# Kernel tuning notes

Measured on AMD Instinct MI355X. Metric: run time of the kernel, lower is better.

Reference implementation:

```python
import jax, jax.numpy as jnp
import numpy as np

B, S, D, H = 2, 2048, 1024, 16
HD = D // H          # 64
NREF = HD // 2       # 32 Householder reflections
BLOCK = 128          # flex_attention block granularity
ROPE_BASE = 10000.0


def setup_inputs() -> dict:
    key = jax.random.key(0)
    ks = jax.random.split(key, 12)
    x = jax.random.normal(ks[0], (B, S, D), jnp.float32)
    # block-causal block mask (flex_attention block_mask analogue)
    nb = S // BLOCK
    bm = jnp.tril(jnp.ones((nb, nb), bool))
    mask = jnp.repeat(jnp.repeat(bm, BLOCK, axis=0), BLOCK, axis=1)  # [S,S]
    s = lambda fan: fan ** -0.5
    vs = jax.random.normal(ks[1], (NREF, HD), jnp.float32) * 0.02
    w_qkv = jax.random.normal(ks[2], (D, 3 * D), jnp.float32) * s(D)
    w_out = jax.random.normal(ks[3], (D, D), jnp.float32) * s(D)
    w_gate = jax.random.normal(ks[4], (D, D), jnp.float32) * s(D)
    b_gate = jnp.zeros((D,), jnp.float32)
    w_mlp_gate = jax.random.normal(ks[5], (D, 8 * D), jnp.float32) * s(D)
    b_mlp_gate = jnp.zeros((8 * D,), jnp.float32)
    w_mlp_out = jax.random.normal(ks[6], (4 * D, D), jnp.float32) * s(4 * D)
    b_mlp_out = jnp.zeros((D,), jnp.float32)
    return dict(x=x, mask=mask, grid_size=S, vs=vs, w_qkv=w_qkv, w_out=w_out,
                w_gate=w_gate, b_gate=b_gate, w_mlp_gate=w_mlp_gate,
                b_mlp_gate=b_mlp_gate, w_mlp_out=w_mlp_out, b_mlp_out=b_mlp_out)


def rmsnorm(x):
    return x * jax.lax.rsqrt(jnp.mean(x * x, axis=-1, keepdims=True) + 1e-6)


def householder_matrix(vs):
    # Q = prod_i (I - 2 v_i v_i^T / |v_i|^2), applied sequentially as in torch loop
    def body(Q, v):
        vn = jnp.sum(v * v) + 1e-8
        return Q - (2.0 / vn) * jnp.outer(v, v @ Q), None
    Q0 = jnp.eye(HD, dtype=vs.dtype)
    Q, _ = jax.lax.scan(body, Q0, vs)
    return Q


def rope_tables(seq_len, dtype):
    inv_freq = 1.0 / (ROPE_BASE ** (jnp.arange(0, HD, 2, dtype=jnp.float32) / HD))
    ang = jnp.arange(seq_len, dtype=jnp.float32)[:, None] * inv_freq  # [S, HD/2]
    ang = jnp.concatenate([ang, ang], axis=-1)                        # [S, HD]
    return jnp.cos(ang).astype(dtype), jnp.sin(ang).astype(dtype)


def rotate_half(x):
    x1, x2 = jnp.split(x, 2, axis=-1)
    return jnp.concatenate([-x2, x1], axis=-1)


def reference(x, mask, grid_size, vs, w_qkv, w_out, w_gate, b_gate,
              w_mlp_gate, b_mlp_gate, w_mlp_out, b_mlp_out):
    del grid_size  # positions derived from sequence length
    resid = x
    h = rmsnorm(x)
    qkv = h @ w_qkv                                # [B,S,3D]
    q, k, v = jnp.split(qkv, 3, axis=-1)
    to_heads = lambda t: t.reshape(B, S, H, HD).transpose(0, 2, 1, 3)  # [B,H,S,hd]
    q, k, v = to_heads(q), to_heads(k), to_heads(v)

    # RnRoPE: inverse Householder rotation, rope, forward Householder rotation
    Q = householder_matrix(vs)                     # [hd,hd]
    q = q @ Q.T
    k = k @ Q.T
    cos, sin = rope_tables(S, x.dtype)             # [S,hd]
    cos = cos[None, None]; sin = sin[None, None]
    q = q * cos + rotate_half(q) * sin
    k = k * cos + rotate_half(k) * sin
    q = q @ Q
    k = k @ Q

    # block-sparse attention (mask realized as boolean [S,S])
    scores = jnp.einsum('bhqd,bhkd->bhqk', q, k) / jnp.sqrt(jnp.asarray(HD, x.dtype))
    scores = jnp.where(mask[None, None], scores, jnp.asarray(-1e30, x.dtype))
    attn = jnp.einsum('bhqk,bhkd->bhqd', jax.nn.softmax(scores, axis=-1), v)
    attn = attn.transpose(0, 2, 1, 3).reshape(B, S, D)
    attn = attn @ w_out

    gate = jax.nn.sigmoid(attn @ w_gate + b_gate)
    x = resid + attn * gate

    resid = x
    gv = rmsnorm(x) @ w_mlp_gate + b_mlp_gate      # [B,S,8D]
    g, val = jnp.split(gv, 2, axis=-1)
    x = resid + (val * jax.nn.gelu(g, approximate=False)) @ w_mlp_out + b_mlp_out
    return x
```

## Files before the change

kernel.cpp:

```cpp
#include <hip/hip_runtime.h>
#include <hip/hip_bf16.h>
#include <math.h>

#define BT 2
#define SEQ 2048
#define DIM 1024
#define NH 16
#define HD 64
#define NTOK (BT*SEQ)

typedef __attribute__((ext_vector_type(4))) float floatx4;
typedef __attribute__((ext_vector_type(8))) short shortx8;
typedef __attribute__((ext_vector_type(4))) short shortx4;

#define GLL16(gp, lp) __builtin_amdgcn_global_load_lds( \
    (const __attribute__((address_space(1))) unsigned int*)(const void*)(gp), \
    (__attribute__((address_space(3))) unsigned int*)(void*)(lp), 16, 0, 0)

__device__ __forceinline__ float bf2f(unsigned short u) {
    unsigned int x = ((unsigned int)u) << 16;
    return __builtin_bit_cast(float, x);
}
__device__ __forceinline__ unsigned short f2bf(float f) {
    unsigned int x = __builtin_bit_cast(unsigned int, f);
    unsigned int lsb = (x >> 16) & 1u;
    x += 0x7fffu + lsb;
    return (unsigned short)(x >> 16);
}
__device__ __forceinline__ float ldin_f(const void* p, size_t i, int isbf) {
    return isbf ? bf2f(((const unsigned short*)p)[i]) : ((const float*)p)[i];
}

__global__ void detect_kernel(const unsigned short* __restrict__ x, int* __restrict__ flag) {
    __shared__ int cnt;
    if (threadIdx.x == 0) cnt = 0;
    __syncthreads();
    unsigned short u = x[(size_t)threadIdx.x * 2];
    int e = (u >> 7) & 0xFF;
    if (e >= 100 && e <= 140) atomicAdd(&cnt, 1);
    __syncthreads();
    if (threadIdx.x == 0) *flag = (cnt >= 192) ? 1 : 0;
}

__global__ void transpose_any(const void* __restrict__ in,
                              unsigned short* __restrict__ out, int R, int C,
                              const int* __restrict__ flagp) {
    int isbf = *flagp;
    __shared__ unsigned short tile[32][33];
    int c0 = blockIdx.x * 32, r0 = blockIdx.y * 32;
    int tx = threadIdx.x, ty = threadIdx.y;
#pragma unroll
    for (int i = 0; i < 4; i++) {
        size_t idx = (size_t)(r0 + ty + i * 8) * C + c0 + tx;
        tile[ty + i * 8][tx] = isbf ? ((const unsigned short*)in)[idx]
                                    : f2bf(((const float*)in)[idx]);
    }
    __syncthreads();
#pragma unroll
    for (int i = 0; i < 4; i++)
        out[(size_t)(c0 + ty + i * 8) * R + r0 + tx] = tile[tx][ty + i * 8];
}

__global__ __launch_bounds__(64) void householder_kernel(const void* __restrict__ vs,
                                                         float* __restrict__ Qg,
                                                         const int* __restrict__ flagp) {
    int isbf = *flagp;
    __shared__ float vsh[64];
    int j = threadIdx.x;
    float Qc[64];
#pragma unroll
    for (int i = 0; i < 64; i++) Qc[i] = (i == j) ? 1.f : 0.f;
    for (int r = 0; r < 32; r++) {
        vsh[j] = ldin_f(vs, r * 64 + j, isbf);
        __syncthreads();
        float va[64];
#pragma unroll
        for (int i = 0; i < 64; i++) va[i] = vsh[i];
        float vn0 = 0.f, vn1 = 0.f, vn2 = 0.f, vn3 = 0.f;
        float t0 = 0.f, t1 = 0.f, t2 = 0.f, t3 = 0.f;
#pragma unroll
        for (int i = 0; i < 16; i++) {
            vn0 += va[4 * i + 0] * va[4 * i + 0];
            vn1 += va[4 * i + 1] * va[4 * i + 1];
            vn2 += va[4 * i + 2] * va[4 * i + 2];
            vn3 += va[4 * i + 3] * va[4 * i + 3];
            t0 += va[4 * i + 0] * Qc[4 * i + 0];
            t1 += va[4 * i + 1] * Qc[4 * i + 1];
            t2 += va[4 * i + 2] * Qc[4 * i + 2];
            t3 += va[4 * i + 3] * Qc[4 * i + 3];
        }
        float vn = (vn0 + vn1) + (vn2 + vn3) + 1e-8f;
        float t = (t0 + t1) + (t2 + t3);
        float c = (2.f / vn) * t;
#pragma unroll
        for (int i = 0; i < 64; i++) Qc[i] -= c * va[i];
        __syncthreads();
    }
#pragma unroll
    for (int i = 0; i < 64; i++) Qg[i * 64 + j] = Qc[i];
}

__global__ __launch_bounds__(256) void rotate_wqkv(unsigned short* __restrict__ wT,
                                                   const float* __restrict__ Qg) {
    __shared__ float Qs[64][64];
    __shared__ unsigned short tile[64][128];
    int bid = blockIdx.x;
    int row0 = (bid >> 3) * 64;
    int col0 = (bid & 7) * 128;
    int t = threadIdx.x;
#pragma unroll
    for (int i = 0; i < 16; i++) {
        int idx = i * 256 + t;
        Qs[idx >> 6][idx & 63] = Qg[idx];
    }
#pragma unroll
    for (int i = 0; i < 8; i++) {
        int e = i * 256 + t;
        int r = e >> 5, cg = (e & 31) * 4;
        *(shortx4*)&tile[r][cg] = *(const shortx4*)&wT[(size_t)(row0 + r) * 1024 + col0 + cg];
    }
    __syncthreads();
    int ib = t >> 5;
    int c = (t & 31) * 4;
    float acc[8][4];
#pragma unroll
    for (int rr = 0; rr < 8; rr++)
#pragma unroll
        for (int cx = 0; cx < 4; cx++) acc[rr][cx] = 0.f;
    for (int j = 0; j < 64; j++) {
        float t0 = bf2f(tile[j][c]);
        float t1 = bf2f(tile[j][c + 1]);
        float t2 = bf2f(tile[j][c + 2]);
        float t3 = bf2f(tile[j][c + 3]);
#pragma unroll
        for (int rr = 0; rr < 8; rr++) {
            float qv = Qs[rr * 8 + ib][j];
            acc[rr][0] += qv * t0;
            acc[rr][1] += qv * t1;
            acc[rr][2] += qv * t2;
            acc[rr][3] += qv * t3;
        }
    }
#pragma unroll
    for (int rr = 0; rr < 8; rr++) {
        int i = rr * 8 + ib;
        shortx4 o4;
#pragma unroll
        for (int cx = 0; cx < 4; cx++) o4[cx] = (short)f2bf(acc[rr][cx]);
        *(shortx4*)&wT[(size_t)(row0 + i) * 1024 + col0 + c] = o4;
    }
}

__global__ void rope_table(float* __restrict__ tab) {
    int idx = blockIdx.x * 256 + threadIdx.x;
    int s = idx >> 5, fi = idx & 31;
    float invf = __expf(-(float)fi * (9.210340371976184f / 32.f));
    float ang = (float)s * invf;
    tab[2 * idx]     = cosf(ang);
    tab[2 * idx + 1] = sinf(ang);
}

__global__ __launch_bounds__(256) void rmsnorm2(const void* __restrict__ x,
                                                unsigned short* __restrict__ h,
                                                const int* __restrict__ flagp) {
    int isbf = flagp ? *flagp : 1;
    __shared__ float red[256];
    int row = blockIdx.x, t = threadIdx.x;
    size_t base = (size_t)row * DIM;
    float v[4];
    float ss = 0.f;
#pragma unroll
    for (int i = 0; i < 4; i++) {
        v[i] = ldin_f(x, base + t + 256 * i, isbf);
        ss += v[i] * v[i];
    }
    red[t] = ss;
    __syncthreads();
    for (int s = 128; s > 0; s >>= 1) {
        if (t < s) red[t] += red[t + s];
        __syncthreads();
    }
    float rs = rsqrtf(red[0] * (1.f / 1024.f) + 1e-6f);
#pragma unroll
    for (int i = 0; i < 4; i++) h[base + t + 256 * i] = f2bf(v[i] * rs);
}

template<int MODE>
__global__ __launch_bounds__(256) void gemm_bt(const unsigned short* __restrict__ A,
                                               const unsigned short* __restrict__ Bt,
                                               void* __restrict__ C,
                                               const void* __restrict__ bias,
                                               const unsigned short* __restrict__ resid,
                                               const void* __restrict__ xin,
                                               const int* __restrict__ flagp,
                                               int M, int N, int K) {
    __shared__ __align__(16) unsigned short As[2][128][64];
    __shared__ __align__(16) unsigned short Bs[2][64][64];
    int isbf = flagp ? *flagp : 1;
    int tile = (blockIdx.x & 7) * (gridDim.x >> 3) + (blockIdx.x >> 3);
    int nbn = N >> 6;
    int m0 = (tile / nbn) * 128;
    int n0 = (tile % nbn) * 64;
    int t = threadIdx.x;
    int lane = t & 63;
    int w = t >> 6;
    int wr = (w >> 1) * 64;
    int wc = (w & 1) * 32;
    int lr = lane & 15;
    int kg = lane >> 4;
    int l8 = lane >> 3, s8 = lane & 7;
    int segswz = (s8 ^ l8) * 8;
    int cs0 = ((kg)     ^ (lr & 7)) * 8;
    int cs1 = ((4 + kg) ^ (lr & 7)) * 8;

    floatx4 acc[4][2];
#pragma unroll
    for (int i = 0; i < 4; i++)
#pragma unroll
        for (int j = 0; j < 2; j++) acc[i][j] = (floatx4){0.f, 0.f, 0.f, 0.f};

    int rbase = w * 8 + l8;
    const unsigned short* aP0 = A + (size_t)(m0 + rbase +  0) * K + segswz;
    const unsigned short* aP1 = A + (size_t)(m0 + rbase + 32) * K + segswz;
    const unsigned short* aP2 = A + (size_t)(m0 + rbase + 64) * K + segswz;
    const unsigned short* aP3 = A + (size_t)(m0 + rbase + 96) * K + segswz;
    const unsigned short* bP0 = Bt + (size_t)(n0 + rbase +  0) * K + segswz;
    const unsigned short* bP1 = Bt + (size_t)(n0 + rbase + 32) * K + segswz;

    auto STAGE = [&](int s, int B) {
        int off = s * 64;
        GLL16(aP0 + off, &As[B][w * 8 +  0][0]);
        GLL16(aP1 + off, &As[B][w * 8 + 32][0]);
        GLL16(aP2 + off, &As[B][w * 8 + 64][0]);
        GLL16(aP3 + off, &As[B][w * 8 + 96][0]);
        GLL16(bP0 + off, &Bs[B][w * 8 +  0][0]);
        GLL16(bP1 + off, &Bs[B][w * 8 + 32][0]);
    };
    auto MM = [&](int B) {
        shortx8 af[4][2], bf[2][2];
#pragma unroll
        for (int i = 0; i < 4; i++) {
            af[i][0] = *(const shortx8*)&As[B][wr + i * 16 + lr][cs0];
            af[i][1] = *(const shortx8*)&As[B][wr + i * 16 + lr][cs1];
        }
#pragma unroll
        for (int j = 0; j < 2; j++) {
            bf[j][0] = *(const shortx8*)&Bs[B][wc + j * 16 + lr][cs0];
            bf[j][1] = *(const shortx8*)&Bs[B][wc + j * 16 + lr][cs1];
        }
#pragma unroll
        for (int i = 0; i < 4; i++)
#pragma unroll
            for (int j = 0; j < 2; j++) {
                acc[i][j] = __builtin_amdgcn_mfma_f32_16x16x32_bf16(af[i][0], bf[j][0], acc[i][j], 0, 0, 0);
                acc[i][j] = __builtin_amdgcn_mfma_f32_16x16x32_bf16(af[i][1], bf[j][1], acc[i][j], 0, 0, 0);
            }
    };

    int NS = K >> 6;
    STAGE(0, 0);
    __syncthreads();
    for (int s = 0; s < NS; s += 2) {
        if (s + 1 < NS) STAGE(s + 1, 1);
        MM(0);
        __syncthreads();
        if (s + 1 < NS) {
            if (s + 2 < NS) STAGE(s + 2, 0);
            MM(1);
            __syncthreads();
        }
    }
#pragma unroll
    for (int i = 0; i < 4; i++) {
#pragma unroll
        for (int j = 0; j < 2; j++) {
            int col = n0 + wc + j * 16 + lr;
            int rb = m0 + wr + i * 16 + kg * 4;
            float bv = bias ? ldin_f(bias, col, isbf) : 0.f;
#pragma unroll
            for (int r = 0; r < 4; r++) {
                float val = acc[i][j][r] + bv;
                size_t oidx = (size_t)(rb + r) * N + col;
                if constexpr (MODE == 0) {
                    ((unsigned short*)C)[oidx] = f2bf(val);
                } else if constexpr (MODE == 1) {
                    ((float*)C)[oidx] = val + bf2f(resid[oidx]);
                } else {
                    float a = bf2f(resid[oidx]);
                    float sg = 1.f / (1.f + __expf(-val));
                    ((unsigned short*)C)[oidx] = f2bf(ldin_f(xin, oidx, isbf) + a * sg);
                }
            }
        }
    }
}

__global__ __launch_bounds__(256) void gemm_glu(const unsigned short* __restrict__ A,
                                                const unsigned short* __restrict__ Bt,
                                                unsigned short* __restrict__ act,
                                                const void* __restrict__ bias,
                                                const int* __restrict__ flagp) {
    __shared__ __align__(16) unsigned short As[2][128][64];
    __shared__ __align__(16) unsigned short Bg[2][64][64];
    __shared__ __align__(16) unsigned short Bv[2][64][64];
    const int K = 1024;
    int isbf = *flagp;
    int tile = (blockIdx.x & 7) * (gridDim.x >> 3) + (blockIdx.x >> 3);
    int m0 = (tile & 31) * 128;
    int n0 = (tile >> 5) * 64;
    int t = threadIdx.x;
    int lane = t & 63;
    int w = t >> 6;
    int wr = (w >> 1) * 64;
    int wc = (w & 1) * 32;
    int lr = lane & 15;
    int kg = lane >> 4;
    int l8 = lane >> 3, s8 = lane & 7;
    int segswz = (s8 ^ l8) * 8;
    int cs0 = ((kg)     ^ (lr & 7)) * 8;
    int cs1 = ((4 + kg) ^ (lr & 7)) * 8;

    floatx4 ag[4][2], av[4][2];
#pragma unroll
    for (int i = 0; i < 4; i++)
#pragma unroll
        for (int j = 0; j < 2; j++) {
            ag[i][j] = (floatx4){0.f, 0.f, 0.f, 0.f};
            av[i][j] = (floatx4){0.f, 0.f, 0.f, 0.f};
        }

    int rbase = w * 8 + l8;
    const unsigned short* aP0 = A + (size_t)(m0 + rbase +  0) * K + segswz;
    const unsigned short* aP1 = A + (size_t)(m0 + rbase + 32) * K + segswz;
    const unsigned short* aP2 = A + (size_t)(m0 + rbase + 64) * K + segswz;
    const unsigned short* aP3 = A + (size_t)(m0 + rbase + 96) * K + segswz;
    const unsigned short* gP0 = Bt + (size_t)(n0 + rbase +  0) * K + segswz;
    const unsigned short* gP1 = Bt + (size_t)(n0 + rbase + 32) * K + segswz;
    const unsigned short* vP0 = Bt + (size_t)(4096 + n0 + rbase +  0) * K + segswz;
    const unsigned short* vP1 = Bt + (size_t)(4096 + n0 + rbase + 32) * K + segswz;

    auto STAGE = [&](int s, int B) {
        int off = s * 64;
        GLL16(aP0 + off, &As[B][w * 8 +  0][0]);
        GLL16(aP1 + off, &As[B][w * 8 + 32][0]);
        GLL16(aP2 + off, &As[B][w * 8 + 64][0]);
        GLL16(aP3 + off, &As[B][w * 8 + 96][0]);
        GLL16(gP0 + off, &Bg[B][w * 8 +  0][0]);
        GLL16(gP1 + off, &Bg[B][w * 8 + 32][0]);
        GLL16(vP0 + off, &Bv[B][w * 8 +  0][0]);
        GLL16(vP1 + off, &Bv[B][w * 8 + 32][0]);
    };
    auto MM = [&](int B) {
        shortx8 af[4][2], gf[2][2], vf[2][2];
#pragma unroll
        for (int i = 0; i < 4; i++) {
            af[i][0] = *(const shortx8*)&As[B][wr + i * 16 + lr][cs0];
            af[i][1] = *(const shortx8*)&As[B][wr + i * 16 + lr][cs1];
        }
#pragma unroll
        for (int j = 0; j < 2; j++) {
            gf[j][0] = *(const shortx8*)&Bg[B][wc + j * 16 + lr][cs0];
            gf[j][1] = *(const shortx8*)&Bg[B][wc + j * 16 + lr][cs1];
            vf[j][0] = *(const shortx8*)&Bv[B][wc + j * 16 + lr][cs0];
            vf[j][1] = *(const shortx8*)&Bv[B][wc + j * 16 + lr][cs1];
        }
#pragma unroll
        for (int i = 0; i < 4; i++)
#pragma unroll
            for (int j = 0; j < 2; j++) {
                ag[i][j] = __builtin_amdgcn_mfma_f32_16x16x32_bf16(af[i][0], gf[j][0], ag[i][j], 0, 0, 0);
                ag[i][j] = __builtin_amdgcn_mfma_f32_16x16x32_bf16(af[i][1], gf[j][1], ag[i][j], 0, 0, 0);
                av[i][j] = __builtin_amdgcn_mfma_f32_16x16x32_bf16(af[i][0], vf[j][0], av[i][j], 0, 0, 0);
                av[i][j] = __builtin_amdgcn_mfma_f32_16x16x32_bf16(af[i][1], vf[j][1], av[i][j], 0, 0, 0);
            }
    };

    const int NS = K >> 6;
    STAGE(0, 0);
    __syncthreads();
    for (int s = 0; s < NS; s += 2) {
        if (s + 1 < NS) STAGE(s + 1, 1);
        MM(0);
        __syncthreads();
        if (s + 1 < NS) {
            if (s + 2 < NS) STAGE(s + 2, 0);
            MM(1);
            __syncthreads();
        }
    }
#pragma unroll
    for (int i = 0; i < 4; i++) {
#pragma unroll
        for (int j = 0; j < 2; j++) {
            int col = n0 + wc + j * 16 + lr;
            int rb = m0 + wr + i * 16 + kg * 4;
            float bgv = ldin_f(bias, col, isbf);
            float bvv = ldin_f(bias, 4096 + col, isbf);
#pragma unroll
            for (int r = 0; r < 4; r++) {
                float g = ag[i][j][r] + bgv;
                float v = av[i][j][r] + bvv;
                float ge = 0.5f * g * (1.f + erff(g * 0.70710678118f));
                act[(size_t)(rb + r) * 4096 + col] = f2bf(v * ge);
            }
        }
    }
}

__global__ __launch_bounds__(256) void qk_rope3(const unsigned short* __restrict__ qkv,
                                                const float* __restrict__ tab,
                                                unsigned short* __restrict__ q_r,
                                                unsigned short* __restrict__ k_r) {
    int tid = blockIdx.x * 256 + threadIdx.x;
    int c = tid & 3;
    int h = (tid >> 2) & 15;
    int ts = tid >> 6;
    int s = ts & 2047, b = ts >> 11;
    int d0 = c * 8;
    const unsigned short* base = qkv + (size_t)ts * 3072 + h * 64;
    shortx8 qlo = *(const shortx8*)(base + d0);
    shortx8 qhi = *(const shortx8*)(base + d0 + 32);
    shortx8 klo = *(const shortx8*)(base + 1024 + d0);
    shortx8 khi = *(const shortx8*)(base + 1024 + d0 + 32);
    const float* tp = tab + (size_t)s * 64 + d0 * 2;
    shortx8 oql, oqh, okl, okh;
#pragma unroll
    for (int i = 0; i < 8; i++) {
        float cv = tp[2 * i], sv = tp[2 * i + 1];
        float ql = bf2f((unsigned short)qlo[i]), qh = bf2f((unsigned short)qhi[i]);
        float kl = bf2f((unsigned short)klo[i]), kh = bf2f((unsigned short)khi[i]);
        oql[i] = (short)f2bf(ql * cv - qh * sv);
        oqh[i] = (short)f2bf(qh * cv + ql * sv);
        okl[i] = (short)f2bf(kl * cv - kh * sv);
        okh[i] = (short)f2bf(kh * cv + kl * sv);
    }
    size_t o = ((size_t)(b * NH + h) * SEQ + s) * HD + d0;
    *(shortx8*)(q_r + o)      = oql;
    *(shortx8*)(q_r + o + 32) = oqh;
    *(shortx8*)(k_r + o)      = okl;
    *(shortx8*)(k_r + o + 32) = okh;
}

__global__ __launch_bounds__(512) void attn_mfma(const unsigned short* __restrict__ q_r,
                                                 const unsigned short* __restrict__ k_r,
                                                 const unsigned short* __restrict__ qkv,
                                                 unsigned short* __restrict__ attn) {
    __shared__ __align__(16) unsigned short Ks[64][72];
    __shared__ __align__(16) unsigned short Vt[64 * 72];
    __shared__ __align__(16) unsigned short Ps[8][16][72];
    int bid = blockIdx.x;
    int qblk = 15 - (bid & 15);
    int bh = bid >> 4;
    int b = bh >> 4, h = bh & 15;
    size_t bh_off = (size_t)bh * SEQ * HD;
    int tid = threadIdx.x;
    int wv = tid >> 6, lane = tid & 63;
    int l16 = lane & 15, quad = lane >> 4;
    int q0 = qblk * 128 + wv * 16;

    const unsigned short* qrow = q_r + bh_off + (size_t)(q0 + l16) * HD + quad * 8;
    shortx8 aq0 = *(const shortx8*)(qrow);
    shortx8 aq1 = *(const shortx8*)(qrow + 32);

    floatx4 o[4];
#pragma unroll
    for (int nt = 0; nt < 4; nt++) o[nt] = (floatx4){0.f, 0.f, 0.f, 0.f};
    float m_run = -1e30f, l_run = 0.f;

    int nk = (qblk + 1) * 128;
    int skey = tid >> 3;
    int sd0 = (tid & 7) * 8;
    const unsigned short* kbase = k_r + bh_off + (size_t)skey * HD + sd0;
    const unsigned short* vbase = qkv + ((size_t)(b * SEQ + skey)) * 3072 + 2048 + h * 64 + sd0;
    int vco = (((skey >> 3) ^ (tid & 7)) * 8) + (skey & 7);

    shortx8 kv = *(const shortx8*)kbase;
    shortx8 vvv = *(const shortx8*)vbase;

    for (int k0 = 0; k0 < nk; k0 += 64) {
        __syncthreads();
        *(shortx8*)&Ks[skey][sd0] = kv;
#pragma unroll
        for (int i = 0; i < 8; i++) Vt[(size_t)(sd0 + i) * 72 + vco] = (unsigned short)vvv[i];
        __syncthreads();
        if (k0 + 64 < nk) {
            kv  = *(const shortx8*)(kbase + (size_t)(k0 + 64) * HD);
            vvv = *(const shortx8*)(vbase + (size_t)(k0 + 64) * 3072);
        }

        floatx4 sc[4];
#pragma unroll
        for (int kt = 0; kt < 4; kt++) {
            shortx8 bk0 = *(const shortx8*)&Ks[kt * 16 + l16][quad * 8];
            shortx8 bk1 = *(const shortx8*)&Ks[kt * 16 + l16][32 + quad * 8];
            floatx4 z = (floatx4){0.f, 0.f, 0.f, 0.f};
            z = __builtin_amdgcn_mfma_f32_16x16x32_bf16(bk0, aq0, z, 0, 0, 0);
            z = __builtin_amdgcn_mfma_f32_16x16x32_bf16(bk1, aq1, z, 0, 0, 0);
            sc[kt] = z;
        }
        float sv[16], mx[16];
#pragma unroll
        for (int kt = 0; kt < 4; kt++)
#pragma unroll
            for (int r = 0; r < 4; r++) sv[kt * 4 + r] = sc[kt][r] * 0.125f;
#pragma unroll
        for (int i = 0; i < 16; i++) mx[i] = sv[i];
#pragma unroll
        for (int st = 8; st > 0; st >>= 1)
#pragma unroll
            for (int i = 0; i < 8; i++)
                if (i < st) mx[i] = fmaxf(mx[i], mx[i + st]);
        float mt = mx[0];
        mt = fmaxf(mt, __shfl_xor(mt, 16, 64));
        mt = fmaxf(mt, __shfl_xor(mt, 32, 64));
        float nm = fmaxf(m_run, mt);
        float al = __expf(m_run - nm);
        m_run = nm;
        float p[16];
#pragma unroll
        for (int i = 0; i < 16; i++) p[i] = __expf(sv[i] - nm);
        float sm[8];
#pragma unroll
        for (int i = 0; i < 8; i++) sm[i] = p[i] + p[i + 8];
        float ps = ((sm[0] + sm[1]) + (sm[2] + sm[3])) + ((sm[4] + sm[5]) + (sm[6] + sm[7]));
        ps += __shfl_xor(ps, 16, 64);
        ps += __shfl_xor(ps, 32, 64);
        l_run = l_run * al + ps;
#pragma unroll
        for (int kt = 0; kt < 4; kt++) {
            shortx4 pk;
#pragma unroll
            for (int r = 0; r < 4; r++) pk[r] = (short)f2bf(p[kt * 4 + r]);
            *(shortx4*)&Ps[wv][l16][kt * 16 + quad * 4] = pk;
        }
#pragma unroll
        for (int r = 0; r < 4; r++) {
            float alr = __shfl(al, quad * 4 + r, 64);
            o[0][r] *= alr; o[1][r] *= alr; o[2][r] *= alr; o[3][r] *= alr;
        }
#pragma unroll
        for (int h2 = 0; h2 < 2; h2++) {
            shortx8 ap = *(const shortx8*)&Ps[wv][l16][h2 * 32 + quad * 8];
#pragma unroll
            for (int nt = 0; nt < 4; nt++) {
                int dd = nt * 16 + l16;
                shortx8 bvv = *(const shortx8*)&Vt[(size_t)dd * 72 +
                                                   (((h2 * 4 + quad) ^ ((dd >> 3) & 7)) * 8)];
                o[nt] = __builtin_amdgcn_mfma_f32_16x16x32_bf16(ap, bvv, o[nt], 0, 0, 0);
            }
        }
    }
#pragma unroll
    for (int r = 0; r < 4; r++) {
        float lv = __shfl(l_run, quad * 4 + r, 64);
        float inv_l = 1.f / lv;
        int s = q0 + quad * 4 + r;
        unsigned short* op = attn + ((size_t)(b * SEQ + s)) * DIM + h * 64;
#pragma unroll
        for (int nt = 0; nt < 4; nt++) op[nt * 16 + l16] = f2bf(o[nt][r] * inv_l);
    }
}

extern "C" void kernel_launch(void* const* d_in, const int* in_sizes, int n_in,
                              void* d_out, int out_size, void* d_ws, size_t ws_size,
                              hipStream_t stream) {
    const unsigned short* x        = (const unsigned short*)d_in[0];
    const void* vs       = d_in[3];
    const void* w_qkv    = d_in[4];
    const void* w_out    = d_in[5];
    const void* w_gate   = d_in[6];
    const void* b_gate   = d_in[7];
    const void* w_mlp_g  = d_in[8];
    const void* b_mlp_g  = d_in[9];
    const void* w_mlp_o  = d_in[10];
    const void* b_mlp_o  = d_in[11];
    float* out = (float*)d_out;
    char* ws = (char*)d_ws;

    if (n_in < 12) return;
    if (in_sizes[0] != 4194304 || in_sizes[3] != 2048 || in_sizes[4] != 3145728 ||
        in_sizes[8] != 8388608 || in_sizes[10] != 4194304 || in_sizes[7] != 1024) return;

    const size_t o_T   = 0;
    const size_t o_Qg  = 35651584;
    const size_t o_h   = 35684352;
    const size_t o_B   = 44072960;
    const size_t o_C   = 69238784;
    const size_t o_gv  = 94404608;
    const size_t total = 161513472;
    if (ws_size < total) return;

    unsigned short* wqkvT  = (unsigned short*)(ws + o_T);
    unsigned short* woutT  = (unsigned short*)(ws + o_T + 6291456);
    unsigned short* wgateT = (unsigned short*)(ws + o_T + 8388608);
    unsigned short* wmgT   = (unsigned short*)(ws + o_T + 10485760);
    unsigned short* wmoT   = (unsigned short*)(ws + o_T + 27262976);
    float*          Qg     = (float*)(ws + o_Qg);
    int*            flagp  = (int*)(ws + o_Qg + 16384);
    unsigned short* h      = (unsigned short*)(ws + o_h);
    unsigned short* qkv    = (unsigned short*)(ws + o_B);
    unsigned short* ao     = (unsigned short*)(ws + o_B + 8388608);
    unsigned short* q_rb   = (unsigned short*)(ws + o_C);
    unsigned short* k_rb   = (unsigned short*)(ws + o_C + 8388608);
    unsigned short* attnb  = (unsigned short*)(ws + o_C + 16777216);
    unsigned short* x1     = (unsigned short*)(ws + o_C);
    unsigned short* act    = (unsigned short*)(ws + o_C + 8388608);
    float*          rtab   = (float*)(ws + o_gv);

    detect_kernel<<<1, 256, 0, stream>>>(x, flagp);
    householder_kernel<<<1, 64, 0, stream>>>(vs, Qg, flagp);
    rope_table<<<256, 256, 0, stream>>>(rtab);

    dim3 tb(32, 8);
    transpose_any<<<dim3(3072 / 32, 1024 / 32), tb, 0, stream>>>(w_qkv,   wqkvT, 1024, 3072, flagp);
    transpose_any<<<dim3(1024 / 32, 1024 / 32), tb, 0, stream>>>(w_out,   woutT, 1024, 1024, flagp);
    transpose_any<<<dim3(1024 / 32, 1024 / 32), tb, 0, stream>>>(w_gate,  wgateT, 1024, 1024, flagp);
    transpose_any<<<dim3(8192 / 32, 1024 / 32), tb, 0, stream>>>(w_mlp_g, wmgT, 1024, 8192, flagp);
    transpose_any<<<dim3(1024 / 32, 4096 / 32), tb, 0, stream>>>(w_mlp_o, wmoT, 4096, 1024, flagp);
    rotate_wqkv<<<256, 256, 0, stream>>>(wqkvT, Qg);

    rmsnorm2<<<NTOK, 256, 0, stream>>>(x, h, flagp);
    gemm_bt<0><<<32 * 48, 256, 0, stream>>>(h, wqkvT, qkv, nullptr, nullptr, nullptr, flagp, NTOK, 3072, 1024);
    qk_rope3<<<1024, 256, 0, stream>>>(qkv, rtab, q_rb, k_rb);
    attn_mfma<<<BT * NH * (SEQ / 128), 512, 0, stream>>>(q_rb, k_rb, qkv, attnb);
    gemm_bt<0><<<32 * 16, 256, 0, stream>>>(attnb, woutT, ao, nullptr, nullptr, nullptr, flagp, NTOK, 1024, 1024);
    gemm_bt<2><<<32 * 16, 256, 0, stream>>>(ao, wgateT, x1, b_gate, ao, x, flagp, NTOK, 1024, 1024);
    rmsnorm2<<<NTOK, 256, 0, stream>>>(x1, h, nullptr);
    gemm_glu<<<32 * 64, 256, 0, stream>>>(h, wmgT, act, b_mlp_g, flagp);
    gemm_bt<1><<<32 * 16, 256, 0, stream>>>(act, wmoT, (void*)out, b_mlp_o, x1, nullptr, flagp, NTOK, 1024, 4096);
}
```

Before: 541.4 us.

## Swizzle GEMM tile order into supergroups, warp-shuffle rmsnorm, prioritize attention MFMA

GEMM and GLU kernels now map block indices into GM x GN supergroups of tiles, so that blocks running at the same time share A and B panels in L2. The rmsnorm reduction swaps the shared-memory tree and its many barriers for a wavefront xor-shuffle plus a single barrier. The attention kernel raises wave priority around its MFMA sections with s_setprio so matrix work can interleave better with softmax in other waves. These target L2 traffic, barrier overhead, and issue scheduling, at the cost of a more complex tile-index mapping that assumes the tile counts divide evenly.

```diff
diff --git a/kernel.cpp b/kernel.cpp
--- a/kernel.cpp
+++ b/kernel.cpp
@@ -164,7 +164,7 @@
                                                 unsigned short* __restrict__ h,
                                                 const int* __restrict__ flagp) {
     int isbf = flagp ? *flagp : 1;
-    __shared__ float red[256];
+    __shared__ float wred[4];
     int row = blockIdx.x, t = threadIdx.x;
     size_t base = (size_t)row * DIM;
     float v[4];
@@ -174,18 +174,17 @@
         v[i] = ldin_f(x, base + t + 256 * i, isbf);
         ss += v[i] * v[i];
     }
-    red[t] = ss;
+#pragma unroll
+    for (int m = 1; m < 64; m <<= 1) ss += __shfl_xor(ss, m, 64);
+    if ((t & 63) == 0) wred[t >> 6] = ss;
     __syncthreads();
-    for (int s = 128; s > 0; s >>= 1) {
-        if (t < s) red[t] += red[t + s];
-        __syncthreads();
-    }
-    float rs = rsqrtf(red[0] * (1.f / 1024.f) + 1e-6f);
+    float tot = (wred[0] + wred[1]) + (wred[2] + wred[3]);
+    float rs = rsqrtf(tot * (1.f / 1024.f) + 1e-6f);
 #pragma unroll
     for (int i = 0; i < 4; i++) h[base + t + 256 * i] = f2bf(v[i] * rs);
 }
 
-template<int MODE>
+template<int MODE, int GM, int GN>
 __global__ __launch_bounds__(256) void gemm_bt(const unsigned short* __restrict__ A,
                                                const unsigned short* __restrict__ Bt,
                                                void* __restrict__ C,
@@ -197,10 +196,13 @@
     __shared__ __align__(16) unsigned short As[2][128][64];
     __shared__ __align__(16) unsigned short Bs[2][64][64];
     int isbf = flagp ? *flagp : 1;
-    int tile = (blockIdx.x & 7) * (gridDim.x >> 3) + (blockIdx.x >> 3);
+    int t0 = (blockIdx.x & 7) * (gridDim.x >> 3) + (blockIdx.x >> 3);
     int nbn = N >> 6;
-    int m0 = (tile / nbn) * 128;
-    int n0 = (tile % nbn) * 64;
+    constexpr int SB = GM * GN;
+    int s0 = t0 / SB, inner = t0 % SB;
+    int sbn = nbn / GN;
+    int m0 = ((s0 / sbn) * GM + (inner % GM)) * 128;
+    int n0 = ((s0 % sbn) * GN + (inner / GM)) * 64;
     int t = threadIdx.x;
     int lane = t & 63;
     int w = t >> 6;
@@ -305,9 +307,10 @@
     __shared__ __align__(16) unsigned short Bv[2][64][64];
     const int K = 1024;
     int isbf = *flagp;
-    int tile = (blockIdx.x & 7) * (gridDim.x >> 3) + (blockIdx.x >> 3);
-    int m0 = (tile & 31) * 128;
-    int n0 = (tile >> 5) * 64;
+    int t0 = (blockIdx.x & 7) * (gridDim.x >> 3) + (blockIdx.x >> 3);
+    int s0 = t0 >> 6, inner = t0 & 63;
+    int m0 = ((s0 >> 3) * 8 + (inner & 7)) * 128;
+    int n0 = ((s0 & 7) * 8 + (inner >> 3)) * 64;
     int t = threadIdx.x;
     int lane = t & 63;
     int w = t >> 6;
@@ -489,6 +492,7 @@
         }
 
         floatx4 sc[4];
+        __builtin_amdgcn_s_setprio(1);
 #pragma unroll
         for (int kt = 0; kt < 4; kt++) {
             shortx8 bk0 = *(const shortx8*)&Ks[kt * 16 + l16][quad * 8];
@@ -498,6 +502,7 @@
             z = __builtin_amdgcn_mfma_f32_16x16x32_bf16(bk1, aq1, z, 0, 0, 0);
             sc[kt] = z;
         }
+        __builtin_amdgcn_s_setprio(0);
         float sv[16], mx[16];
 #pragma unroll
         for (int kt = 0; kt < 4; kt++)
@@ -538,6 +543,7 @@
             float alr = __shfl(al, quad * 4 + r, 64);
             o[0][r] *= alr; o[1][r] *= alr; o[2][r] *= alr; o[3][r] *= alr;
         }
+        __builtin_amdgcn_s_setprio(1);
 #pragma unroll
         for (int h2 = 0; h2 < 2; h2++) {
             shortx8 ap = *(const shortx8*)&Ps[wv][l16][h2 * 32 + quad * 8];
@@ -549,6 +555,7 @@
                 o[nt] = __builtin_amdgcn_mfma_f32_16x16x32_bf16(ap, bvv, o[nt], 0, 0, 0);
             }
         }
+        __builtin_amdgcn_s_setprio(0);
     }
 #pragma unroll
     for (int r = 0; r < 4; r++) {
@@ -620,12 +627,12 @@
     rotate_wqkv<<<256, 256, 0, stream>>>(wqkvT, Qg);
 
     rmsnorm2<<<NTOK, 256, 0, stream>>>(x, h, flagp);
-    gemm_bt<0><<<32 * 48, 256, 0, stream>>>(h, wqkvT, qkv, nullptr, nullptr, nullptr, flagp, NTOK, 3072, 1024);
+    gemm_bt<0, 4, 8><<<32 * 48, 256, 0, stream>>>(h, wqkvT, qkv, nullptr, nullptr, nullptr, flagp, NTOK, 3072, 1024);
     qk_rope3<<<1024, 256, 0, stream>>>(qkv, rtab, q_rb, k_rb);
     attn_mfma<<<BT * NH * (SEQ / 128), 512, 0, stream>>>(q_rb, k_rb, qkv, attnb);
-    gemm_bt<0><<<32 * 16, 256, 0, stream>>>(attnb, woutT, ao, nullptr, nullptr, nullptr, flagp, NTOK, 1024, 1024);
-    gemm_bt<2><<<32 * 16, 256, 0, stream>>>(ao, wgateT, x1, b_gate, ao, x, flagp, NTOK, 1024, 1024);
+    gemm_bt<0, 4, 8><<<32 * 16, 256, 0, stream>>>(attnb, woutT, ao, nullptr, nullptr, nullptr, flagp, NTOK, 1024, 1024);
+    gemm_bt<2, 4, 8><<<32 * 16, 256, 0, stream>>>(ao, wgateT, x1, b_gate, ao, x, flagp, NTOK, 1024, 1024);
     rmsnorm2<<<NTOK, 256, 0, stream>>>(x1, h, nullptr);
     gemm_glu<<<32 * 64, 256, 0, stream>>>(h, wmgT, act, b_mlp_g, flagp);
-    gemm_bt<1><<<32 * 16, 256, 0, stream>>>(act, wmoT, (void*)out, b_mlp_o, x1, nullptr, flagp, NTOK, 1024, 4096);
-}
+    gemm_bt<1, 2, 4><<<32 * 16, 256, 0, stream>>>(act, wmoT, (void*)out, b_mlp_o, x1, nullptr, flagp, NTOK, 1024, 4096);
+}
```

New measurement: 540.7 us. No clear change (-0.1%).
